# Performance work log

Hardware: AMD Instinct MI355X
Metric: run time of the kernel (lower is better)

Reference implementation:

```python
import jax, jax.numpy as jnp
import numpy as np

B, T_OUT, C, L = 8, 8, 64, 1024  # batch, temporal channels, spatial channels (=in_channels), time steps


def setup_inputs() -> dict:
    key = jax.random.key(0)
    ks = jax.random.split(key, 7)
    s = 1.0 / np.sqrt(C)  # conv1d default init scale
    return {
        "x": jax.random.normal(ks[0], (B, T_OUT, C, L), dtype=jnp.float32),
        "Wq": jax.random.uniform(ks[1], (C, C), jnp.float32, -s, s),
        "bq": jax.random.uniform(ks[2], (C,), jnp.float32, -s, s),
        "Wk": jax.random.uniform(ks[3], (C, C), jnp.float32, -s, s),
        "bk": jax.random.uniform(ks[4], (C,), jnp.float32, -s, s),
        "Wv": jax.random.uniform(ks[5], (C, C), jnp.float32, -s, s),
        "bv": jax.random.uniform(ks[6], (C,), jnp.float32, -s, s),
    }


def reference(x, Wq, bq, Wk, bk, Wv, bv):
    b, t, c, l = x.shape
    xr = x.reshape(b * t, c, l)  # [BT, C, L]
    # 1x1 Conv1d == per-timestep linear over channels
    q = jnp.einsum('oc,bcl->bol', Wq, xr) + bq[:, None]
    k = jnp.einsum('oc,bcl->bol', Wk, xr) + bk[:, None]
    v = jnp.einsum('oc,bcl->bol', Wv, xr) + bv[:, None]
    # scores[b, i, j] = sum_c q[b, c, i] * k[b, c, j]  -> [BT, L, L]
    scores = jnp.einsum('bci,bcj->bij', q, k)
    weights = jax.nn.softmax(scores, axis=-1)
    # out[b, i, c] = sum_j weights[b, i, j] * v[b, c, j]
    out = jnp.einsum('bij,bcj->bic', weights, v)
    out = jnp.transpose(out, (0, 2, 1))  # [BT, C, L]
    return out.reshape(b, t, c, l)
```

## Files before the change

kernel.cpp:

```cpp
#include <hip/hip_runtime.h>

#define CC 64
#define LL 1024
#define LOG2E 1.44269504f

typedef unsigned short u16;
typedef unsigned int u32;
typedef __attribute__((ext_vector_type(8))) short short8;
typedef __attribute__((ext_vector_type(4))) float floatx4;

static __device__ __forceinline__ u16 f2b(float f) {
  return (u16)((__float_as_uint(f) + 0x8000u) >> 16);
}
static __device__ __forceinline__ u32 pk2(float a, float b) {
  return ((__float_as_uint(a) + 0x8000u) >> 16) |
         ((__float_as_uint(b) + 0x8000u) & 0xffff0000u);
}
static __device__ __forceinline__ u32 pk2t(float a, float b) {
  return __builtin_amdgcn_perm(__float_as_uint(b), __float_as_uint(a), 0x07060302u);
}
static __device__ __forceinline__ short8 mk8(u32 a, u32 b, u32 c, u32 d) {
  union { u32 u[4]; short8 s; } t;
  t.u[0] = a; t.u[1] = b; t.u[2] = c; t.u[3] = d;
  return t.s;
}

__global__ __launch_bounds__(256) void w_prep(
    const float* __restrict__ Wq, const float* __restrict__ bq,
    const float* __restrict__ Wk, const float* __restrict__ bk,
    const float* __restrict__ Wv, const float* __restrict__ bv,
    u16* __restrict__ whi, float* __restrict__ bsc)
{
  const int idx = blockIdx.x * 256 + threadIdx.x;
  const int m = idx >> 12;
  const float* W = (m == 0) ? Wq : (m == 1) ? Wk : Wv;
  const float w = W[idx & 4095] * ((m == 0) ? LOG2E : 1.0f);
  whi[idx] = f2b(w);
  if (blockIdx.x == 0 && threadIdx.x < 192)
    bsc[threadIdx.x] = (threadIdx.x < 64) ? bq[threadIdx.x] * LOG2E
                     : (threadIdx.x < 128) ? bk[threadIdx.x - 64] : bv[threadIdx.x - 128];
}

__global__ __launch_bounds__(256) void qkv_kernel(
    const float* __restrict__ x,
    const u16* __restrict__ whi, const float* __restrict__ bsc,
    u16* __restrict__ qT, u16* __restrict__ kT, u16* __restrict__ vO)
{
  __shared__ __align__(16) u16 xh_s[64 * 72];
  __shared__ __align__(16) u16 tbuf_s[4 * 16 * 72];
  __shared__ float b_s[192];

  const int tid  = threadIdx.x;
  const int wave = tid >> 6;
  const int lane = tid & 63;
  const int l16  = lane & 15;
  const int quad = lane >> 4;

  const int bt = blockIdx.x & 63;
  const int l0 = (blockIdx.x >> 6) << 6;

  const int lx = tid & 63;
  const int cg = (tid >> 6) << 4;
  const float* xp = x + ((size_t)bt * CC + cg) * LL + l0 + lx;

  float v0[16];
  #pragma unroll
  for (int e = 0; e < 16; ++e) v0[e] = xp[(size_t)e * LL];
  if (tid < 192) b_s[tid] = bsc[tid];
  #pragma unroll
  for (int e = 0; e < 16; e += 2)
    *(u32*)(xh_s + lx * 72 + cg + e) = pk2(v0[e], v0[e + 1]);
  __syncthreads();

  const u16* xr_h = xh_s + (wave * 16 + l16) * 72 + quad * 8;
  const short8 xh0 = *(const short8*)(xr_h);
  const short8 xh1 = *(const short8*)(xr_h + 32);

  u16* tb = tbuf_s + wave * 1152;

  #pragma unroll
  for (int ot = 0; ot < 12; ++ot) {
    const int m = ot >> 2;
    const int off = (m << 12) + (((ot & 3) * 16 + l16) << 6) + quad * 8;
    const short8 ah0 = *(const short8*)(whi + off);
    const short8 ah1 = *(const short8*)(whi + off + 32);

    floatx4 acc = (floatx4){0.f, 0.f, 0.f, 0.f};
    acc = __builtin_amdgcn_mfma_f32_16x16x32_bf16(ah0, xh0, acc, 0, 0, 0);
    acc = __builtin_amdgcn_mfma_f32_16x16x32_bf16(ah1, xh1, acc, 0, 0, 0);

    float ov[4];
    #pragma unroll
    for (int r = 0; r < 4; ++r)
      ov[r] = acc[r] + b_s[ot * 16 + quad * 4 + r];

    if (ot < 8) {
      uint2 pv;
      pv.x = pk2(ov[0], ov[1]);
      pv.y = pk2(ov[2], ov[3]);
      *(uint2*)(tb + l16 * 72 + (ot & 3) * 16 + quad * 4) = pv;
      if ((ot & 3) == 3) {
        asm volatile("" ::: "memory");
        u16* gdst = ((ot < 4) ? qT : kT) + ((size_t)(bt * LL + l0 + wave * 16)) * CC;
        const int rr = lane >> 3;
        const int c8 = (lane & 7) * 8;
        #pragma unroll
        for (int s2 = 0; s2 < 2; ++s2) {
          const int row = s2 * 8 + rr;
          uint4 val = *(const uint4*)(tb + row * 72 + c8);
          *(uint4*)(gdst + row * CC + c8) = val;
        }
        asm volatile("" ::: "memory");
      }
    } else {
      const int ob = (ot - 8) * 16 + quad * 4;
      u16* vdst = vO + ((size_t)(bt * CC + ob)) * LL + l0 + wave * 16 + l16;
      #pragma unroll
      for (int r = 0; r < 4; ++r)
        vdst[(size_t)r * LL] = f2b(ov[r]);
    }
  }
}

__global__ __launch_bounds__(256) void attn_kernel(
    const u16* __restrict__ qT, const u16* __restrict__ kT,
    const u16* __restrict__ vB, float* __restrict__ out)
{
  __shared__ __align__(16) u16 smem[18432];
  const int tid  = threadIdx.x;
  const int wave = tid >> 6;
  const int lane = tid & 63;
  const int l16  = lane & 15;
  const int quad = lane >> 4;

  const int bt    = blockIdx.x & 63;
  const int chunk = blockIdx.x >> 6;
  const int i0w   = (chunk << 6) + (wave << 4);

  const u16* kbase = kT + (size_t)bt * LL * CC;
  const u16* vbase = vB + (size_t)bt * CC * LL;

  short8 qf[2];
  {
    const u16* qr = qT + (size_t)bt * LL * CC + (size_t)(i0w + l16) * CC + quad * 8;
    qf[0] = *(const short8*)(qr);
    qf[1] = *(const short8*)(qr + 32);
  }

  floatx4 O[4];
  #pragma unroll
  for (int cf = 0; cf < 4; ++cf)
    O[cf] = (floatx4){0.f, 0.f, 0.f, 0.f};
  float lsA = 0.f, lsB = 0.f;

  const int r_st = tid >> 2;
  const int c_st = (tid & 3) << 4;
  const int sr = (r_st & 0x20) | ((r_st & 4) << 2) | ((r_st & 0x18) >> 1) | (r_st & 3);

  {
    uint4 k0 = *(const uint4*)(kbase + (size_t)r_st * CC + c_st);
    uint4 k1 = *(const uint4*)(kbase + (size_t)r_st * CC + c_st + 8);
    uint4 v0 = *(const uint4*)(vbase + (size_t)r_st * LL + c_st);
    uint4 v1 = *(const uint4*)(vbase + (size_t)r_st * LL + c_st + 8);
    *(uint4*)(smem + sr * 72 + c_st)              = k0;
    *(uint4*)(smem + sr * 72 + c_st + 8)          = k1;
    *(uint4*)(smem + 4608 + r_st * 72 + c_st)     = v0;
    *(uint4*)(smem + 4608 + r_st * 72 + c_st + 8) = v1;
  }
  __syncthreads();

  for (int it = 0; it < 16; ++it) {
    u16* ktc = smem + (it & 1) * 9216;
    u16* vtc = ktc + 4608;

    uint4 rk0, rk1, rv0, rv1;
    if (it < 15) {
      const int jb = (it + 1) << 6;
      rk0 = *(const uint4*)(kbase + (size_t)(jb + r_st) * CC + c_st);
      rk1 = *(const uint4*)(kbase + (size_t)(jb + r_st) * CC + c_st + 8);
      rv0 = *(const uint4*)(vbase + (size_t)r_st * LL + jb + c_st);
      rv1 = *(const uint4*)(vbase + (size_t)r_st * LL + jb + c_st + 8);
      __builtin_amdgcn_sched_barrier(0);
    }

    floatx4 S[4];
    __builtin_amdgcn_s_setprio(1);
    #pragma unroll
    for (int jt = 0; jt < 4; ++jt) {
      const u16* ka = ktc + (jt * 16 + l16) * 72 + quad * 8;
      const short8 a0 = *(const short8*)(ka);
      const short8 a1 = *(const short8*)(ka + 32);
      floatx4 acc = (floatx4){0.f, 0.f, 0.f, 0.f};
      acc = __builtin_amdgcn_mfma_f32_16x16x32_bf16(a0, qf[0], acc, 0, 0, 0);
      acc = __builtin_amdgcn_mfma_f32_16x16x32_bf16(a1, qf[1], acc, 0, 0, 0);
      S[jt] = acc;
    }
    __builtin_amdgcn_s_setprio(0);

    short8 v0f[4], v1f[4];
    #pragma unroll
    for (int cf = 0; cf < 4; ++cf) {
      const u16* va = vtc + (cf * 16 + l16) * 72 + quad * 8;
      v0f[cf] = *(const short8*)(va);
      v1f[cf] = *(const short8*)(va + 32);
    }

    uint2 pp[4];
    #pragma unroll
    for (int jt = 0; jt < 4; ++jt) {
      const float e0 = __builtin_amdgcn_exp2f(S[jt][0]);
      const float e1 = __builtin_amdgcn_exp2f(S[jt][1]);
      const float e2 = __builtin_amdgcn_exp2f(S[jt][2]);
      const float e3 = __builtin_amdgcn_exp2f(S[jt][3]);
      lsA += e0 + e1;
      lsB += e2 + e3;
      pp[jt].x = pk2t(e0, e1);
      pp[jt].y = pk2t(e2, e3);
    }

    __builtin_amdgcn_s_setprio(1);
    {
      const short8 pa0 = mk8(pp[0].x, pp[0].y, pp[1].x, pp[1].y);
      const short8 pa1 = mk8(pp[2].x, pp[2].y, pp[3].x, pp[3].y);
      #pragma unroll
      for (int cf = 0; cf < 4; ++cf) {
        O[cf] = __builtin_amdgcn_mfma_f32_16x16x32_bf16(pa0, v0f[cf], O[cf], 0, 0, 0);
        O[cf] = __builtin_amdgcn_mfma_f32_16x16x32_bf16(pa1, v1f[cf], O[cf], 0, 0, 0);
      }
    }
    __builtin_amdgcn_s_setprio(0);

    if (it < 15) {
      u16* ktn = smem + ((it + 1) & 1) * 9216;
      *(uint4*)(ktn + sr * 72 + c_st)              = rk0;
      *(uint4*)(ktn + sr * 72 + c_st + 8)          = rk1;
      *(uint4*)(ktn + 4608 + r_st * 72 + c_st)     = rv0;
      *(uint4*)(ktn + 4608 + r_st * 72 + c_st + 8) = rv1;
    }
    __syncthreads();
  }

  float lsum = lsA + lsB;
  lsum += __shfl_xor(lsum, 16, 64);
  lsum += __shfl_xor(lsum, 32, 64);

  __syncthreads();
  float* of = (float*)smem + wave * 1280;
  #pragma unroll
  for (int r = 0; r < 4; ++r) {
    const float rl = __builtin_amdgcn_rcpf(__shfl(lsum, quad * 4 + r, 64));
    #pragma unroll
    for (int cf = 0; cf < 4; ++cf)
      O[cf][r] *= rl;
  }
  asm volatile("" ::: "memory");
  #pragma unroll
  for (int cf = 0; cf < 4; ++cf)
    #pragma unroll
    for (int r = 0; r < 4; ++r)
      of[(cf * 16 + l16) * 20 + quad * 4 + r] = O[cf][r];
  asm volatile("" ::: "memory");
  {
    float* ob = out + ((size_t)bt * CC) * LL + i0w;
    #pragma unroll
    for (int rr = 0; rr < 4; ++rr) {
      const int c = rr * 16 + l16;
      float4 val = *(const float4*)(of + c * 20 + quad * 4);
      *(float4*)(ob + (size_t)c * LL + quad * 4) = val;
    }
  }
  asm volatile("" ::: "memory");
}

extern "C" void kernel_launch(void* const* d_in, const int* in_sizes, int n_in,
                              void* d_out, int out_size, void* d_ws, size_t ws_size,
                              hipStream_t stream) {
  const float* x  = (const float*)d_in[0];
  const float* Wq = (const float*)d_in[1];
  const float* bq = (const float*)d_in[2];
  const float* Wk = (const float*)d_in[3];
  const float* bk = (const float*)d_in[4];
  const float* Wv = (const float*)d_in[5];
  const float* bv = (const float*)d_in[6];
  float* out = (float*)d_out;

  u16* qTp = (u16*)d_ws;
  u16* kTp = qTp + (size_t)64 * LL * CC;
  u16* vp  = kTp + (size_t)64 * LL * CC;
  u16* whi = vp  + (size_t)64 * LL * CC;
  float* bsc = (float*)(whi + 3 * 64 * 64);

  w_prep<<<48, 256, 0, stream>>>(Wq, bq, Wk, bk, Wv, bv, whi, bsc);
  qkv_kernel<<<1024, 256, 0, stream>>>(x, whi, bsc, qTp, kTp, vp);
  attn_kernel<<<1024, 256, 0, stream>>>(qTp, kTp, vp, out);
}
```

Measured before the change: 122.8 us.

## Split attention keys across waves with cross-wave output reduction

Each wave now handles all 64 query rows of the block against its own 16-key slice of each tile, where before each wave owned 16 query rows against all keys. Partial outputs and row sums are combined through shared memory, using plain stores from two waves and LDS atomicAdds from the other two, before the final normalisation and store. The aim is to stop every wave from re-reading the full K and V tiles from shared memory and to batch more MFMAs per fragment load. The price is a larger accumulator register footprint (O[4][4]), a reduction step at the end of the block, and a launch-bounds occupancy hint.

```diff
diff --git a/kernel.cpp b/kernel.cpp
--- a/kernel.cpp
+++ b/kernel.cpp
@@ -122,7 +122,7 @@
   }
 }
 
-__global__ __launch_bounds__(256) void attn_kernel(
+__global__ __launch_bounds__(256, 3) void attn_kernel(
     const u16* __restrict__ qT, const u16* __restrict__ kT,
     const u16* __restrict__ vB, float* __restrict__ out)
 {
@@ -135,141 +135,213 @@
 
   const int bt    = blockIdx.x & 63;
   const int chunk = blockIdx.x >> 6;
-  const int i0w   = (chunk << 6) + (wave << 4);
+  const int i0b   = chunk << 6;
 
   const u16* kbase = kT + (size_t)bt * LL * CC;
   const u16* vbase = vB + (size_t)bt * CC * LL;
 
-  short8 qf[2];
-  {
-    const u16* qr = qT + (size_t)bt * LL * CC + (size_t)(i0w + l16) * CC + quad * 8;
-    qf[0] = *(const short8*)(qr);
-    qf[1] = *(const short8*)(qr + 32);
-  }
-
-  floatx4 O[4];
-  #pragma unroll
-  for (int cf = 0; cf < 4; ++cf)
-    O[cf] = (floatx4){0.f, 0.f, 0.f, 0.f};
-  float lsA = 0.f, lsB = 0.f;
+  short8 qf[4][2];
+  #pragma unroll
+  for (int it4 = 0; it4 < 4; ++it4) {
+    const u16* qr = qT + (size_t)bt * LL * CC + (size_t)(i0b + it4 * 16 + l16) * CC + quad * 8;
+    qf[it4][0] = *(const short8*)(qr);
+    qf[it4][1] = *(const short8*)(qr + 32);
+  }
+
+  floatx4 O[4][4];
+  #pragma unroll
+  for (int a = 0; a < 4; ++a)
+    #pragma unroll
+    for (int b = 0; b < 4; ++b)
+      O[a][b] = (floatx4){0.f, 0.f, 0.f, 0.f};
+  float ls[4] = {0.f, 0.f, 0.f, 0.f};
 
   const int r_st = tid >> 2;
   const int c_st = (tid & 3) << 4;
-  const int sr = (r_st & 0x20) | ((r_st & 4) << 2) | ((r_st & 0x18) >> 1) | (r_st & 3);
 
   {
     uint4 k0 = *(const uint4*)(kbase + (size_t)r_st * CC + c_st);
     uint4 k1 = *(const uint4*)(kbase + (size_t)r_st * CC + c_st + 8);
     uint4 v0 = *(const uint4*)(vbase + (size_t)r_st * LL + c_st);
     uint4 v1 = *(const uint4*)(vbase + (size_t)r_st * LL + c_st + 8);
-    *(uint4*)(smem + sr * 72 + c_st)              = k0;
-    *(uint4*)(smem + sr * 72 + c_st + 8)          = k1;
-    *(uint4*)(smem + 4608 + r_st * 72 + c_st)     = v0;
-    *(uint4*)(smem + 4608 + r_st * 72 + c_st + 8) = v1;
+    *(uint4*)(smem + r_st * 72 + c_st)              = k0;
+    *(uint4*)(smem + r_st * 72 + c_st + 8)          = k1;
+    *(uint4*)(smem + 4608 + r_st * 72 + c_st)       = v0;
+    *(uint4*)(smem + 4608 + r_st * 72 + c_st + 8)   = v1;
   }
   __syncthreads();
 
-  for (int it = 0; it < 16; ++it) {
-    u16* ktc = smem + (it & 1) * 9216;
-    u16* vtc = ktc + 4608;
-
-    uint4 rk0, rk1, rv0, rv1;
-    if (it < 15) {
-      const int jb = (it + 1) << 6;
-      rk0 = *(const uint4*)(kbase + (size_t)(jb + r_st) * CC + c_st);
-      rk1 = *(const uint4*)(kbase + (size_t)(jb + r_st) * CC + c_st + 8);
-      rv0 = *(const uint4*)(vbase + (size_t)r_st * LL + jb + c_st);
-      rv1 = *(const uint4*)(vbase + (size_t)r_st * LL + jb + c_st + 8);
-      __builtin_amdgcn_sched_barrier(0);
+  const int krd = (wave * 16 + l16) * 72 + quad * 8;
+  const int vrd = l16 * 72 + wave * 16 + quad * 4;
+
+  uint2 vA[4];
+  uint2 ppE[4];
+
+  for (int itp = 0; itp < 8; ++itp) {
+    {
+      const int jb = (2 * itp + 1) << 6;
+      uint4 rk0 = *(const uint4*)(kbase + (size_t)(jb + r_st) * CC + c_st);
+      uint4 rk1 = *(const uint4*)(kbase + (size_t)(jb + r_st) * CC + c_st + 8);
+      uint4 rv0 = *(const uint4*)(vbase + (size_t)r_st * LL + jb + c_st);
+      uint4 rv1 = *(const uint4*)(vbase + (size_t)r_st * LL + jb + c_st + 8);
+
+      const u16* kt = smem;
+      const short8 a0 = *(const short8*)(kt + krd);
+      const short8 a1 = *(const short8*)(kt + krd + 32);
+      floatx4 S[4];
+      __builtin_amdgcn_s_setprio(1);
+      #pragma unroll
+      for (int it4 = 0; it4 < 4; ++it4) {
+        floatx4 acc = (floatx4){0.f, 0.f, 0.f, 0.f};
+        acc = __builtin_amdgcn_mfma_f32_16x16x32_bf16(a0, qf[it4][0], acc, 0, 0, 0);
+        acc = __builtin_amdgcn_mfma_f32_16x16x32_bf16(a1, qf[it4][1], acc, 0, 0, 0);
+        S[it4] = acc;
+      }
+      __builtin_amdgcn_s_setprio(0);
+
+      const u16* vt = smem + 4608;
+      #pragma unroll
+      for (int ct = 0; ct < 4; ++ct)
+        vA[ct] = *(const uint2*)(vt + ct * 1152 + vrd);
+
+      #pragma unroll
+      for (int it4 = 0; it4 < 4; ++it4) {
+        const float e0 = __builtin_amdgcn_exp2f(S[it4][0]);
+        const float e1 = __builtin_amdgcn_exp2f(S[it4][1]);
+        const float e2 = __builtin_amdgcn_exp2f(S[it4][2]);
+        const float e3 = __builtin_amdgcn_exp2f(S[it4][3]);
+        ls[it4] += (e0 + e1) + (e2 + e3);
+        ppE[it4].x = pk2t(e0, e1);
+        ppE[it4].y = pk2t(e2, e3);
+      }
+
+      *(uint4*)(smem + 9216 + r_st * 72 + c_st)             = rk0;
+      *(uint4*)(smem + 9216 + r_st * 72 + c_st + 8)         = rk1;
+      *(uint4*)(smem + 13824 + r_st * 72 + c_st)            = rv0;
+      *(uint4*)(smem + 13824 + r_st * 72 + c_st + 8)        = rv1;
+      __syncthreads();
     }
-
-    floatx4 S[4];
-    __builtin_amdgcn_s_setprio(1);
-    #pragma unroll
-    for (int jt = 0; jt < 4; ++jt) {
-      const u16* ka = ktc + (jt * 16 + l16) * 72 + quad * 8;
-      const short8 a0 = *(const short8*)(ka);
-      const short8 a1 = *(const short8*)(ka + 32);
-      floatx4 acc = (floatx4){0.f, 0.f, 0.f, 0.f};
-      acc = __builtin_amdgcn_mfma_f32_16x16x32_bf16(a0, qf[0], acc, 0, 0, 0);
-      acc = __builtin_amdgcn_mfma_f32_16x16x32_bf16(a1, qf[1], acc, 0, 0, 0);
-      S[jt] = acc;
+    {
+      const bool pf = (itp < 7);
+      uint4 rk0, rk1, rv0, rv1;
+      if (pf) {
+        const int jb = (2 * itp + 2) << 6;
+        rk0 = *(const uint4*)(kbase + (size_t)(jb + r_st) * CC + c_st);
+        rk1 = *(const uint4*)(kbase + (size_t)(jb + r_st) * CC + c_st + 8);
+        rv0 = *(const uint4*)(vbase + (size_t)r_st * LL + jb + c_st);
+        rv1 = *(const uint4*)(vbase + (size_t)r_st * LL + jb + c_st + 8);
+      }
+
+      const u16* kt = smem + 9216;
+      const short8 a0 = *(const short8*)(kt + krd);
+      const short8 a1 = *(const short8*)(kt + krd + 32);
+      floatx4 S[4];
+      __builtin_amdgcn_s_setprio(1);
+      #pragma unroll
+      for (int it4 = 0; it4 < 4; ++it4) {
+        floatx4 acc = (floatx4){0.f, 0.f, 0.f, 0.f};
+        acc = __builtin_amdgcn_mfma_f32_16x16x32_bf16(a0, qf[it4][0], acc, 0, 0, 0);
+        acc = __builtin_amdgcn_mfma_f32_16x16x32_bf16(a1, qf[it4][1], acc, 0, 0, 0);
+        S[it4] = acc;
+      }
+      __builtin_amdgcn_s_setprio(0);
+
+      const u16* vt = smem + 13824;
+      uint2 vC[4];
+      #pragma unroll
+      for (int ct = 0; ct < 4; ++ct)
+        vC[ct] = *(const uint2*)(vt + ct * 1152 + vrd);
+
+      uint2 ppO[4];
+      #pragma unroll
+      for (int it4 = 0; it4 < 4; ++it4) {
+        const float e0 = __builtin_amdgcn_exp2f(S[it4][0]);
+        const float e1 = __builtin_amdgcn_exp2f(S[it4][1]);
+        const float e2 = __builtin_amdgcn_exp2f(S[it4][2]);
+        const float e3 = __builtin_amdgcn_exp2f(S[it4][3]);
+        ls[it4] += (e0 + e1) + (e2 + e3);
+        ppO[it4].x = pk2t(e0, e1);
+        ppO[it4].y = pk2t(e2, e3);
+      }
+
+      short8 vb[4];
+      #pragma unroll
+      for (int ct = 0; ct < 4; ++ct)
+        vb[ct] = mk8(vA[ct].x, vA[ct].y, vC[ct].x, vC[ct].y);
+
+      __builtin_amdgcn_s_setprio(1);
+      #pragma unroll
+      for (int it4 = 0; it4 < 4; ++it4) {
+        const short8 pa = mk8(ppE[it4].x, ppE[it4].y, ppO[it4].x, ppO[it4].y);
+        #pragma unroll
+        for (int ct = 0; ct < 4; ++ct)
+          O[it4][ct] = __builtin_amdgcn_mfma_f32_16x16x32_bf16(pa, vb[ct], O[it4][ct], 0, 0, 0);
+      }
+      __builtin_amdgcn_s_setprio(0);
+
+      if (pf) {
+        *(uint4*)(smem + r_st * 72 + c_st)            = rk0;
+        *(uint4*)(smem + r_st * 72 + c_st + 8)        = rk1;
+        *(uint4*)(smem + 4608 + r_st * 72 + c_st)     = rv0;
+        *(uint4*)(smem + 4608 + r_st * 72 + c_st + 8) = rv1;
+      }
+      __syncthreads();
     }
-    __builtin_amdgcn_s_setprio(0);
-
-    short8 v0f[4], v1f[4];
-    #pragma unroll
-    for (int cf = 0; cf < 4; ++cf) {
-      const u16* va = vtc + (cf * 16 + l16) * 72 + quad * 8;
-      v0f[cf] = *(const short8*)(va);
-      v1f[cf] = *(const short8*)(va + 32);
+  }
+
+  #pragma unroll
+  for (int it4 = 0; it4 < 4; ++it4) {
+    ls[it4] += __shfl_xor(ls[it4], 16, 64);
+    ls[it4] += __shfl_xor(ls[it4], 32, 64);
+  }
+
+  float* red  = (float*)smem;
+  float* redB = red + 4352;
+  float* lss  = red + 8704;
+
+  if (wave < 2) {
+    float* dst = wave ? redB : red;
+    #pragma unroll
+    for (int it4 = 0; it4 < 4; ++it4)
+      #pragma unroll
+      for (int ct = 0; ct < 4; ++ct)
+        *(floatx4*)(dst + (ct * 16 + l16) * 68 + it4 * 16 + quad * 4) = O[it4][ct];
+  }
+  {
+    const float lsv = (quad == 0) ? ls[0] : (quad == 1) ? ls[1] : (quad == 2) ? ls[2] : ls[3];
+    lss[wave * 64 + quad * 16 + l16] = lsv;
+  }
+  __syncthreads();
+
+  if (wave >= 2) {
+    float* dst = (wave == 3) ? redB : red;
+    #pragma unroll
+    for (int it4 = 0; it4 < 4; ++it4)
+      #pragma unroll
+      for (int ct = 0; ct < 4; ++ct)
+        #pragma unroll
+        for (int r = 0; r < 4; ++r)
+          atomicAdd(&dst[(ct * 16 + l16) * 68 + it4 * 16 + quad * 4 + r], O[it4][ct][r]);
+  }
+  if (tid < 64) {
+    const float s = lss[tid] + lss[64 + tid] + lss[128 + tid] + lss[192 + tid];
+    lss[tid] = __builtin_amdgcn_rcpf(s);
+  }
+  __syncthreads();
+
+  {
+    const int c  = tid >> 2;
+    const int kk = tid & 3;
+    float* ob = out + ((size_t)(bt * CC + c)) * LL + i0b + kk * 16;
+    #pragma unroll
+    for (int e = 0; e < 4; ++e) {
+      floatx4 o  = *(const floatx4*)(red  + c * 68 + kk * 16 + e * 4);
+      floatx4 o2 = *(const floatx4*)(redB + c * 68 + kk * 16 + e * 4);
+      floatx4 rl = *(const floatx4*)(lss + kk * 16 + e * 4);
+      o = (o + o2) * rl;
+      *(floatx4*)(ob + e * 4) = o;
     }
-
-    uint2 pp[4];
-    #pragma unroll
-    for (int jt = 0; jt < 4; ++jt) {
-      const float e0 = __builtin_amdgcn_exp2f(S[jt][0]);
-      const float e1 = __builtin_amdgcn_exp2f(S[jt][1]);
-      const float e2 = __builtin_amdgcn_exp2f(S[jt][2]);
-      const float e3 = __builtin_amdgcn_exp2f(S[jt][3]);
-      lsA += e0 + e1;
-      lsB += e2 + e3;
-      pp[jt].x = pk2t(e0, e1);
-      pp[jt].y = pk2t(e2, e3);
-    }
-
-    __builtin_amdgcn_s_setprio(1);
-    {
-      const short8 pa0 = mk8(pp[0].x, pp[0].y, pp[1].x, pp[1].y);
-      const short8 pa1 = mk8(pp[2].x, pp[2].y, pp[3].x, pp[3].y);
-      #pragma unroll
-      for (int cf = 0; cf < 4; ++cf) {
-        O[cf] = __builtin_amdgcn_mfma_f32_16x16x32_bf16(pa0, v0f[cf], O[cf], 0, 0, 0);
-        O[cf] = __builtin_amdgcn_mfma_f32_16x16x32_bf16(pa1, v1f[cf], O[cf], 0, 0, 0);
-      }
-    }
-    __builtin_amdgcn_s_setprio(0);
-
-    if (it < 15) {
-      u16* ktn = smem + ((it + 1) & 1) * 9216;
-      *(uint4*)(ktn + sr * 72 + c_st)              = rk0;
-      *(uint4*)(ktn + sr * 72 + c_st + 8)          = rk1;
-      *(uint4*)(ktn + 4608 + r_st * 72 + c_st)     = rv0;
-      *(uint4*)(ktn + 4608 + r_st * 72 + c_st + 8) = rv1;
-    }
-    __syncthreads();
-  }
-
-  float lsum = lsA + lsB;
-  lsum += __shfl_xor(lsum, 16, 64);
-  lsum += __shfl_xor(lsum, 32, 64);
-
-  __syncthreads();
-  float* of = (float*)smem + wave * 1280;
-  #pragma unroll
-  for (int r = 0; r < 4; ++r) {
-    const float rl = __builtin_amdgcn_rcpf(__shfl(lsum, quad * 4 + r, 64));
-    #pragma unroll
-    for (int cf = 0; cf < 4; ++cf)
-      O[cf][r] *= rl;
-  }
-  asm volatile("" ::: "memory");
-  #pragma unroll
-  for (int cf = 0; cf < 4; ++cf)
-    #pragma unroll
-    for (int r = 0; r < 4; ++r)
-      of[(cf * 16 + l16) * 20 + quad * 4 + r] = O[cf][r];
-  asm volatile("" ::: "memory");
-  {
-    float* ob = out + ((size_t)bt * CC) * LL + i0w;
-    #pragma unroll
-    for (int rr = 0; rr < 4; ++rr) {
-      const int c = rr * 16 + l16;
-      float4 val = *(const float4*)(of + c * 20 + quad * 4);
-      *(float4*)(ob + (size_t)c * LL + quad * 4) = val;
-    }
-  }
-  asm volatile("" ::: "memory");
+  }
 }
 
 extern "C" void kernel_launch(void* const* d_in, const int* in_sizes, int n_in,
```

New measurement: 232.6 us. 1.89x slower.
